# Optimization experiments

Hardware: AMD Instinct MI355X
Metric: run time of the kernel (lower is better)

Reference implementation:

```python
import jax, jax.numpy as jnp
import numpy as np

STD_MIN = 1e-05
MAX_VAL = 100.0

B, T, C = 16, 8192, 128


def setup_inputs() -> dict:
    key = jax.random.key(0)
    k1, k2 = jax.random.split(key)
    x = jax.random.normal(k1, (B, T, C), dtype=jnp.float32)
    # binary missing-value mask (1 = missing), stored as float per mask.float() in torch
    mask = jax.random.randint(k2, (B, T, C), 0, 2).astype(jnp.float32)
    return {"x": x, "mask": mask}


def reference(x, mask):
    # valid-count running along time: n_t = cumsum(1 - mask)
    nm = 1.0 - mask                      # [B,T,C], 1 where observed
    n = jnp.cumsum(nm, axis=1)
    n = jnp.where(n == 0, 1.0, n)        # avoid div-by-zero before first valid point
    # causal running mean (note: cumsum of x includes masked entries, as in original)
    mean = jax.lax.stop_gradient(jnp.cumsum(x, axis=1) / n)
    # causal running std over masked squared deviations
    std = jnp.sqrt(jnp.cumsum(((x - mean) * nm) ** 2, axis=1) / n)
    std = jnp.where(std > STD_MIN, std, 1.0)
    std = jax.lax.stop_gradient(std)
    return jnp.clip((x - mean) / std, -MAX_VAL, MAX_VAL)
```

## Files before the change

kernel.cpp:

```cpp
#include <hip/hip_runtime.h>
#include <math.h>
#include <stdint.h>

constexpr int B = 16;
constexpr int T = 8192;
constexpr int C = 128;
constexpr int CG = C / 4;
constexpr int TBK = 128;
constexpr int NCH = T / TBK;
constexpr int SUBS = 8;
constexpr int RPT = TBK / SUBS;
constexpr float STD_MIN = 1e-5f;
constexpr float MAX_VAL = 100.0f;

using f32x4 = __attribute__((ext_vector_type(4))) float;

__device__ inline f32x4 max1(f32x4 n) {
    f32x4 r;
    #pragma unroll
    for (int j = 0; j < 4; ++j) r[j] = fmaxf(n[j], 1.0f);
    return r;
}
__device__ inline f32x4 rcp4(f32x4 a) {
    f32x4 r;
    #pragma unroll
    for (int j = 0; j < 4; ++j) r[j] = __builtin_amdgcn_rcpf(a[j]);
    return r;
}
__device__ inline f32x4 sqrt4(f32x4 a) {
    f32x4 r;
    #pragma unroll
    for (int j = 0; j < 4; ++j) r[j] = __builtin_amdgcn_sqrtf(a[j]);
    return r;
}
__device__ inline f32x4 decode_nib(unsigned nib) {
    f32x4 r;
    r[0] = (float)(nib & 1u);
    r[1] = (float)((nib >> 1) & 1u);
    r[2] = (float)((nib >> 2) & 1u);
    r[3] = (float)((nib >> 3) & 1u);
    return r;
}

__global__ __launch_bounds__(256) void k1_sums(
    const f32x4* __restrict__ x, const f32x4* __restrict__ mask,
    f32x4* __restrict__ aggx, f32x4* __restrict__ aggn,
    f32x4* __restrict__ subx, f32x4* __restrict__ subn,
    uint64_t* __restrict__ nmw)
{
    __shared__ f32x4 p0[SUBS][CG], p1[SUBS][CG];
    int tid = threadIdx.x, cg = tid & 31, sub = tid >> 5;
    int blk = blockIdx.x, b = blk >> 6, k = blk & (NCH - 1);
    size_t base = ((size_t)b * T + (size_t)k * TBK + (size_t)sub * RPT) * CG + cg;

    f32x4 sx = {0,0,0,0}, sn = {0,0,0,0};
    uint64_t w = 0;
    #pragma unroll
    for (int r = 0; r < RPT; ++r) {
        f32x4 xv = x[base + (size_t)r * CG];
        f32x4 mv = mask[base + (size_t)r * CG];
        f32x4 nm = 1.0f - mv;
        sx += xv; sn += nm;
        unsigned nib = (unsigned)nm[0] | ((unsigned)nm[1] << 1)
                     | ((unsigned)nm[2] << 2) | ((unsigned)nm[3] << 3);
        w |= (uint64_t)nib << (4 * r);
    }
    nmw[(size_t)blk * 256 + tid] = w;
    size_t so = ((size_t)blk * SUBS + sub) * CG + cg;
    subx[so] = sx;
    subn[so] = sn;
    p0[sub][cg] = sx; p1[sub][cg] = sn;
    __syncthreads();
    if (sub == 0) {
        f32x4 tx = p0[0][cg], tn = p1[0][cg];
        #pragma unroll
        for (int s = 1; s < SUBS; ++s) { tx += p0[s][cg]; tn += p1[s][cg]; }
        aggx[(size_t)blk * CG + cg] = tx;
        aggn[(size_t)blk * CG + cg] = tn;
    }
}

__global__ __launch_bounds__(256) void k2_dev2(
    const f32x4* __restrict__ x,
    const f32x4* __restrict__ aggx, const f32x4* __restrict__ aggn,
    const f32x4* __restrict__ subx, const f32x4* __restrict__ subn,
    const uint64_t* __restrict__ nmw,
    f32x4* __restrict__ aggd, f32x4* __restrict__ subd)
{
    __shared__ f32x4 p0[SUBS][CG], p1[SUBS][CG];
    int tid = threadIdx.x, cg = tid & 31, sub = tid >> 5;
    int blk = blockIdx.x, b = blk >> 6, k = blk & (NCH - 1);
    size_t base = ((size_t)b * T + (size_t)k * TBK + (size_t)sub * RPT) * CG + cg;

    f32x4 pxp = {0,0,0,0}, pnp = {0,0,0,0};
    for (int j = sub; j < k; j += SUBS) {
        size_t o = ((size_t)(b * NCH + j)) * CG + cg;
        pxp += aggx[o]; pnp += aggn[o];
    }
    p0[sub][cg] = pxp; p1[sub][cg] = pnp;
    __syncthreads();
    f32x4 px = p0[0][cg], pn = p1[0][cg];
    #pragma unroll
    for (int s = 1; s < SUBS; ++s) { px += p0[s][cg]; pn += p1[s][cg]; }

    f32x4 offx = {0,0,0,0}, offn = {0,0,0,0};
    for (int s = 0; s < sub; ++s) {
        size_t so = ((size_t)blk * SUBS + s) * CG + cg;
        offx += subx[so]; offn += subn[so];
    }
    f32x4 rx = px + offx, rn = pn + offn;
    uint64_t w = nmw[(size_t)blk * 256 + tid];

    f32x4 sd = {0,0,0,0};
    #pragma unroll
    for (int r = 0; r < RPT; ++r) {
        f32x4 xv = x[base + (size_t)r * CG];
        f32x4 nm = decode_nib((unsigned)(w >> (4 * r)) & 0xFu);
        rx += xv; rn += nm;
        f32x4 mean = rx * rcp4(max1(rn));
        f32x4 d = (xv - mean) * nm;
        sd += d * d;
    }
    subd[((size_t)blk * SUBS + sub) * CG + cg] = sd;
    __syncthreads();
    p0[sub][cg] = sd;
    __syncthreads();
    if (sub == 0) {
        f32x4 td = p0[0][cg];
        #pragma unroll
        for (int s = 1; s < SUBS; ++s) td += p0[s][cg];
        aggd[(size_t)blk * CG + cg] = td;
    }
}

__global__ __launch_bounds__(256) void k3_final(
    const f32x4* __restrict__ x,
    const f32x4* __restrict__ aggx, const f32x4* __restrict__ aggn,
    const f32x4* __restrict__ aggd,
    const f32x4* __restrict__ subx, const f32x4* __restrict__ subn,
    const f32x4* __restrict__ subd,
    const uint64_t* __restrict__ nmw, f32x4* __restrict__ out)
{
    __shared__ f32x4 p0[SUBS][CG], p1[SUBS][CG], p2[SUBS][CG];
    int tid = threadIdx.x, cg = tid & 31, sub = tid >> 5;
    int blk = blockIdx.x, b = blk >> 6, k = blk & (NCH - 1);
    size_t base = ((size_t)b * T + (size_t)k * TBK + (size_t)sub * RPT) * CG + cg;

    f32x4 pxp = {0,0,0,0}, pnp = {0,0,0,0}, pdp = {0,0,0,0};
    for (int j = sub; j < k; j += SUBS) {
        size_t o = ((size_t)(b * NCH + j)) * CG + cg;
        pxp += aggx[o]; pnp += aggn[o]; pdp += aggd[o];
    }
    p0[sub][cg] = pxp; p1[sub][cg] = pnp; p2[sub][cg] = pdp;
    __syncthreads();
    f32x4 px = p0[0][cg], pn = p1[0][cg], pd = p2[0][cg];
    #pragma unroll
    for (int s = 1; s < SUBS; ++s) {
        px += p0[s][cg]; pn += p1[s][cg]; pd += p2[s][cg];
    }

    f32x4 offx = {0,0,0,0}, offn = {0,0,0,0}, offd = {0,0,0,0};
    for (int s = 0; s < sub; ++s) {
        size_t so = ((size_t)blk * SUBS + s) * CG + cg;
        offx += subx[so]; offn += subn[so]; offd += subd[so];
    }
    f32x4 rx = px + offx, rn = pn + offn, rd = pd + offd;
    uint64_t w = nmw[(size_t)blk * 256 + tid];

    #pragma unroll
    for (int r = 0; r < RPT; ++r) {
        f32x4 xv = x[base + (size_t)r * CG];
        f32x4 nm = decode_nib((unsigned)(w >> (4 * r)) & 0xFu);
        rx += xv; rn += nm;
        f32x4 inv = rcp4(max1(rn));
        f32x4 mean = rx * inv;
        f32x4 d = (xv - mean) * nm;
        rd += d * d;
        f32x4 s = sqrt4(rd * inv);
        f32x4 ov;
        #pragma unroll
        for (int j = 0; j < 4; ++j) {
            float invs = (s[j] > STD_MIN) ? __builtin_amdgcn_rcpf(s[j]) : 1.0f;
            float v = (xv[j] - mean[j]) * invs;
            ov[j] = fminf(fmaxf(v, -MAX_VAL), MAX_VAL);
        }
        __builtin_nontemporal_store(ov, &out[base + (size_t)r * CG]);
    }
}

extern "C" void kernel_launch(void* const* d_in, const int* in_sizes, int n_in,
                              void* d_out, int out_size, void* d_ws, size_t ws_size,
                              hipStream_t stream) {
    const f32x4* x    = (const f32x4*)d_in[0];
    const f32x4* mask = (const f32x4*)d_in[1];
    f32x4* out = (f32x4*)d_out;

    size_t agg_elems = (size_t)B * NCH * CG;
    size_t sub_elems = (size_t)B * NCH * SUBS * CG;
    f32x4* aggx = (f32x4*)d_ws;
    f32x4* aggn = aggx + agg_elems;
    f32x4* aggd = aggn + agg_elems;
    f32x4* subx = aggd + agg_elems;
    f32x4* subn = subx + sub_elems;
    f32x4* subd = subn + sub_elems;
    uint64_t* nmw = (uint64_t*)(subd + sub_elems);

    int grid = B * NCH;

    k1_sums<<<grid, 256, 0, stream>>>(x, mask, aggx, aggn, subx, subn, nmw);
    k2_dev2<<<grid, 256, 0, stream>>>(x, aggx, aggn, subx, subn, nmw, aggd, subd);
    k3_final<<<grid, 256, 0, stream>>>(x, aggx, aggn, aggd, subx, subn, subd, nmw, out);
}
```

Before: 70.54 us.

## Fuse deviation and final passes via decoupled lookback with ticketed blocks

Merges the second and third kernels into one. Each block takes a dynamic ticket, computes its chunk's squared-deviation sum, publishes it with a release flag, then spin-waits on earlier chunks' flags to get the prefix before writing outputs. The block's x values are kept in registers so x is read from memory once instead of twice across the two passes, and one launch and the subd buffer go away. The cost is serialization through flag polling and higher register pressure from holding 16 f32x4 values per thread.

Measured after the change: 226.6 us. 3.21x slower.

```diff
diff --git a/kernel.cpp b/kernel.cpp
--- a/kernel.cpp
+++ b/kernel.cpp
@@ -10,6 +10,7 @@
 constexpr int NCH = T / TBK;
 constexpr int SUBS = 8;
 constexpr int RPT = TBK / SUBS;
+constexpr int NBLK = B * NCH;
 constexpr float STD_MIN = 1e-5f;
 constexpr float MAX_VAL = 100.0f;
 
@@ -46,12 +47,21 @@
     const f32x4* __restrict__ x, const f32x4* __restrict__ mask,
     f32x4* __restrict__ aggx, f32x4* __restrict__ aggn,
     f32x4* __restrict__ subx, f32x4* __restrict__ subn,
-    uint64_t* __restrict__ nmw)
+    uint64_t* __restrict__ nmw, unsigned* __restrict__ flags,
+    unsigned* __restrict__ ticket)
 {
     __shared__ f32x4 p0[SUBS][CG], p1[SUBS][CG];
     int tid = threadIdx.x, cg = tid & 31, sub = tid >> 5;
     int blk = blockIdx.x, b = blk >> 6, k = blk & (NCH - 1);
     size_t base = ((size_t)b * T + (size_t)k * TBK + (size_t)sub * RPT) * CG + cg;
+
+    if (tid == 0) {
+        __hip_atomic_store(&flags[blk], 0u, __ATOMIC_RELAXED,
+                           __HIP_MEMORY_SCOPE_AGENT);
+        if (blk == 0)
+            __hip_atomic_store(ticket, 0u, __ATOMIC_RELAXED,
+                               __HIP_MEMORY_SCOPE_AGENT);
+    }
 
     f32x4 sx = {0,0,0,0}, sn = {0,0,0,0};
     uint64_t w = 0;
@@ -80,16 +90,24 @@
     }
 }
 
-__global__ __launch_bounds__(256) void k2_dev2(
+__global__ __launch_bounds__(256) void k23_fused(
     const f32x4* __restrict__ x,
     const f32x4* __restrict__ aggx, const f32x4* __restrict__ aggn,
     const f32x4* __restrict__ subx, const f32x4* __restrict__ subn,
     const uint64_t* __restrict__ nmw,
-    f32x4* __restrict__ aggd, f32x4* __restrict__ subd)
+    float* __restrict__ aggd,
+    unsigned* __restrict__ flags, unsigned* __restrict__ ticket,
+    f32x4* __restrict__ out)
 {
     __shared__ f32x4 p0[SUBS][CG], p1[SUBS][CG];
+    __shared__ int s_ticket;
     int tid = threadIdx.x, cg = tid & 31, sub = tid >> 5;
-    int blk = blockIdx.x, b = blk >> 6, k = blk & (NCH - 1);
+
+    if (tid == 0)
+        s_ticket = (int)__hip_atomic_fetch_add(ticket, 1u, __ATOMIC_RELAXED,
+                                               __HIP_MEMORY_SCOPE_AGENT);
+    __syncthreads();
+    int blk = s_ticket, b = blk >> 6, k = blk & (NCH - 1);
     size_t base = ((size_t)b * T + (size_t)k * TBK + (size_t)sub * RPT) * CG + cg;
 
     f32x4 pxp = {0,0,0,0}, pnp = {0,0,0,0};
@@ -108,80 +126,75 @@
         size_t so = ((size_t)blk * SUBS + s) * CG + cg;
         offx += subx[so]; offn += subn[so];
     }
-    f32x4 rx = px + offx, rn = pn + offn;
+    f32x4 rx0 = px + offx, rn0 = pn + offn;
     uint64_t w = nmw[(size_t)blk * 256 + tid];
 
-    f32x4 sd = {0,0,0,0};
+    f32x4 xr[RPT];
+    f32x4 rx = rx0, rn = rn0, sd = {0,0,0,0};
     #pragma unroll
     for (int r = 0; r < RPT; ++r) {
         f32x4 xv = x[base + (size_t)r * CG];
+        xr[r] = xv;
         f32x4 nm = decode_nib((unsigned)(w >> (4 * r)) & 0xFu);
         rx += xv; rn += nm;
         f32x4 mean = rx * rcp4(max1(rn));
         f32x4 d = (xv - mean) * nm;
         sd += d * d;
     }
-    subd[((size_t)blk * SUBS + sub) * CG + cg] = sd;
     __syncthreads();
     p0[sub][cg] = sd;
     __syncthreads();
+    f32x4 offd = {0,0,0,0};
+    for (int s = 0; s < sub; ++s) offd += p0[s][cg];
     if (sub == 0) {
         f32x4 td = p0[0][cg];
         #pragma unroll
         for (int s = 1; s < SUBS; ++s) td += p0[s][cg];
-        aggd[(size_t)blk * CG + cg] = td;
-    }
-}
-
-__global__ __launch_bounds__(256) void k3_final(
-    const f32x4* __restrict__ x,
-    const f32x4* __restrict__ aggx, const f32x4* __restrict__ aggn,
-    const f32x4* __restrict__ aggd,
-    const f32x4* __restrict__ subx, const f32x4* __restrict__ subn,
-    const f32x4* __restrict__ subd,
-    const uint64_t* __restrict__ nmw, f32x4* __restrict__ out)
-{
-    __shared__ f32x4 p0[SUBS][CG], p1[SUBS][CG], p2[SUBS][CG];
-    int tid = threadIdx.x, cg = tid & 31, sub = tid >> 5;
-    int blk = blockIdx.x, b = blk >> 6, k = blk & (NCH - 1);
-    size_t base = ((size_t)b * T + (size_t)k * TBK + (size_t)sub * RPT) * CG + cg;
-
-    f32x4 pxp = {0,0,0,0}, pnp = {0,0,0,0}, pdp = {0,0,0,0};
+        float* dst = &aggd[(size_t)blk * C + cg * 4];
+        #pragma unroll
+        for (int j = 0; j < 4; ++j)
+            __hip_atomic_store(&dst[j], td[j], __ATOMIC_RELAXED,
+                               __HIP_MEMORY_SCOPE_AGENT);
+    }
+    __syncthreads();
+    if (tid == 0)
+        __hip_atomic_store(&flags[blk], 1u, __ATOMIC_RELEASE,
+                           __HIP_MEMORY_SCOPE_AGENT);
+
+    f32x4 pdp = {0,0,0,0};
     for (int j = sub; j < k; j += SUBS) {
-        size_t o = ((size_t)(b * NCH + j)) * CG + cg;
-        pxp += aggx[o]; pnp += aggn[o]; pdp += aggd[o];
-    }
-    p0[sub][cg] = pxp; p1[sub][cg] = pnp; p2[sub][cg] = pdp;
-    __syncthreads();
-    f32x4 px = p0[0][cg], pn = p1[0][cg], pd = p2[0][cg];
-    #pragma unroll
-    for (int s = 1; s < SUBS; ++s) {
-        px += p0[s][cg]; pn += p1[s][cg]; pd += p2[s][cg];
-    }
-
-    f32x4 offx = {0,0,0,0}, offn = {0,0,0,0}, offd = {0,0,0,0};
-    for (int s = 0; s < sub; ++s) {
-        size_t so = ((size_t)blk * SUBS + s) * CG + cg;
-        offx += subx[so]; offn += subn[so]; offd += subd[so];
-    }
-    f32x4 rx = px + offx, rn = pn + offn, rd = pd + offd;
-    uint64_t w = nmw[(size_t)blk * 256 + tid];
-
+        int pb = b * NCH + j;
+        while (__hip_atomic_load(&flags[pb], __ATOMIC_ACQUIRE,
+                                 __HIP_MEMORY_SCOPE_AGENT) == 0u)
+            __builtin_amdgcn_s_sleep(1);
+        const float* src = &aggd[(size_t)pb * C + cg * 4];
+        #pragma unroll
+        for (int jj = 0; jj < 4; ++jj)
+            pdp[jj] += __hip_atomic_load(&src[jj], __ATOMIC_RELAXED,
+                                         __HIP_MEMORY_SCOPE_AGENT);
+    }
+    p1[sub][cg] = pdp;
+    __syncthreads();
+    f32x4 pd = p1[0][cg];
+    #pragma unroll
+    for (int s = 1; s < SUBS; ++s) pd += p1[s][cg];
+    f32x4 rd = pd + offd;
+
+    rx = rx0; rn = rn0;
     #pragma unroll
     for (int r = 0; r < RPT; ++r) {
-        f32x4 xv = x[base + (size_t)r * CG];
         f32x4 nm = decode_nib((unsigned)(w >> (4 * r)) & 0xFu);
-        rx += xv; rn += nm;
+        rx += xr[r]; rn += nm;
         f32x4 inv = rcp4(max1(rn));
         f32x4 mean = rx * inv;
-        f32x4 d = (xv - mean) * nm;
+        f32x4 d = (xr[r] - mean) * nm;
         rd += d * d;
         f32x4 s = sqrt4(rd * inv);
         f32x4 ov;
         #pragma unroll
         for (int j = 0; j < 4; ++j) {
             float invs = (s[j] > STD_MIN) ? __builtin_amdgcn_rcpf(s[j]) : 1.0f;
-            float v = (xv[j] - mean[j]) * invs;
+            float v = (xr[r][j] - mean[j]) * invs;
             ov[j] = fminf(fmaxf(v, -MAX_VAL), MAX_VAL);
         }
         __builtin_nontemporal_store(ov, &out[base + (size_t)r * CG]);
@@ -195,19 +208,19 @@
     const f32x4* mask = (const f32x4*)d_in[1];
     f32x4* out = (f32x4*)d_out;
 
-    size_t agg_elems = (size_t)B * NCH * CG;
-    size_t sub_elems = (size_t)B * NCH * SUBS * CG;
+    size_t agg_elems = (size_t)NBLK * CG;
+    size_t sub_elems = (size_t)NBLK * SUBS * CG;
     f32x4* aggx = (f32x4*)d_ws;
     f32x4* aggn = aggx + agg_elems;
-    f32x4* aggd = aggn + agg_elems;
-    f32x4* subx = aggd + agg_elems;
+    float* aggd = (float*)(aggn + agg_elems);
+    f32x4* subx = (f32x4*)(aggd + (size_t)NBLK * C);
     f32x4* subn = subx + sub_elems;
-    f32x4* subd = subn + sub_elems;
-    uint64_t* nmw = (uint64_t*)(subd + sub_elems);
-
-    int grid = B * NCH;
-
-    k1_sums<<<grid, 256, 0, stream>>>(x, mask, aggx, aggn, subx, subn, nmw);
-    k2_dev2<<<grid, 256, 0, stream>>>(x, aggx, aggn, subx, subn, nmw, aggd, subd);
-    k3_final<<<grid, 256, 0, stream>>>(x, aggx, aggn, aggd, subx, subn, subd, nmw, out);
-}
+    uint64_t* nmw = (uint64_t*)(subn + sub_elems);
+    unsigned* flags  = (unsigned*)(nmw + (size_t)NBLK * 256);
+    unsigned* ticket = flags + NBLK;
+
+    k1_sums<<<NBLK, 256, 0, stream>>>(x, mask, aggx, aggn, subx, subn,
+                                      nmw, flags, ticket);
+    k23_fused<<<NBLK, 256, 0, stream>>>(x, aggx, aggn, subx, subn, nmw,
+                                        aggd, flags, ticket, out);
+}
```
